# Kernel optimization log

Hardware: AMD Instinct MI355X
Metric: run time of the kernel (lower is better)

## Reference

```python
import jax, jax.numpy as jnp
import numpy as np

D_MODEL = 1024
NUM_HEADS = 16
D_K = D_MODEL // NUM_HEADS
THETA = 10000.0
B, S = 2, 2048
MAX_LEN = 2048


def precompute_cos_sin(head_dim, max_len, theta):
    # (max_len, head_dim): first half cos, second half sin, over head_dim//2 freqs
    freqs = 1.0 / theta ** (jnp.arange(0, head_dim, 2, dtype=jnp.float32) / head_dim)
    ang = jnp.arange(max_len, dtype=jnp.float32)[:, None] * freqs[None, :]  # (L, d/2)
    return jnp.concatenate([jnp.cos(ang), jnp.sin(ang)], axis=-1)  # (L, d)


def apply_rope(x, cos_sin):
    # x: (b, h, s, d); cos_sin: (b, 1, s, d) with cos|sin halves of size d//2
    x1 = x[..., 0::2]
    x2 = x[..., 1::2]
    cos, sin = jnp.split(cos_sin, 2, axis=-1)
    out = jnp.stack([x1 * cos - x2 * sin, x1 * sin + x2 * cos], axis=-1)
    return out.reshape(x.shape)


def setup_inputs() -> dict:
    key = jax.random.key(0)
    ks = jax.random.split(key, 6)
    std = np.sqrt(2.0 / (D_MODEL + D_MODEL))
    x = jax.random.normal(ks[0], (B, S, D_MODEL), dtype=jnp.float32)
    token_positions = jnp.sort(
        jax.random.randint(ks[1], (B, S), 0, MAX_LEN, dtype=jnp.int32), axis=-1)
    Wq = jax.random.normal(ks[2], (D_MODEL, D_MODEL), dtype=jnp.float32) * std
    Wk = jax.random.normal(ks[3], (D_MODEL, D_MODEL), dtype=jnp.float32) * std
    Wv = jax.random.normal(ks[4], (D_MODEL, D_MODEL), dtype=jnp.float32) * std
    Wo = jax.random.normal(ks[5], (D_MODEL, D_MODEL), dtype=jnp.float32) * std
    return {"x": x, "token_positions": token_positions,
            "Wq": Wq, "Wk": Wk, "Wv": Wv, "Wo": Wo}


def reference(x, token_positions, Wq, Wk, Wv, Wo):
    b, s, d = x.shape
    h, dk = NUM_HEADS, D_K
    # projections: weight is (out, in)
    Q = jnp.einsum('btd,od->bto', x, Wq).reshape(b, s, h, dk).transpose(0, 2, 1, 3)
    K = jnp.einsum('btd,od->bto', x, Wk).reshape(b, s, h, dk).transpose(0, 2, 1, 3)
    V = jnp.einsum('btd,od->bto', x, Wv).reshape(b, s, h, dk).transpose(0, 2, 1, 3)
    # RoPE
    cos_sin = precompute_cos_sin(dk, MAX_LEN, THETA)  # (L, dk)
    cs = cos_sin[token_positions][:, None, :, :]  # (b, 1, s, dk)
    Q = apply_rope(Q, cs)
    K = apply_rope(K, cs)
    # causal attention with full score matrix, as in the original
    scores = jnp.einsum('bhqd,bhkd->bhqk', Q, K) / jnp.sqrt(jnp.float32(dk))
    causal = jnp.tril(jnp.ones((s, s), dtype=bool))
    scores = jnp.where(causal[None, None], scores, -jnp.inf)
    weights = jax.nn.softmax(scores, axis=-1)
    out = jnp.einsum('bhqk,bhkd->bhqd', weights, V)
    out = out.transpose(0, 2, 1, 3).reshape(b, s, h * dk)
    return jnp.einsum('btd,od->bto', out, Wo)
```

## Files before the change

kernel.cpp:

```cpp
#include <hip/hip_runtime.h>
#include <math.h>

#define D_MODEL 1024
#define NHEADS  16
#define DK      64
#define BB      2
#define SS      2048
#define MT      (BB*SS)

typedef _Float16 half8 __attribute__((ext_vector_type(8)));
typedef _Float16 half4 __attribute__((ext_vector_type(4)));
typedef float f32x4 __attribute__((ext_vector_type(4)));

__global__ void rope_table_kernel(float* __restrict__ tab) {
    int idx = blockIdx.x * 256 + threadIdx.x;
    int p = idx >> 5;
    int i = idx & 31;
    float freq = powf(10000.0f, -(float)(2 * i) / 64.0f);
    float ang = (float)p * freq;
    tab[p * 64 + i]      = cosf(ang);
    tab[p * 64 + 32 + i] = sinf(ang);
}

__global__ __launch_bounds__(256) void gemm_awt_f16(
    const float* __restrict__ A,
    const float* __restrict__ W0, const float* __restrict__ W1, const float* __restrict__ W2,
    float* __restrict__ C0, float* __restrict__ C1, float* __restrict__ C2)
{
    const float* W;
    float* C;
    if (blockIdx.z == 0)      { W = W0; C = C0; }
    else if (blockIdx.z == 1) { W = W1; C = C1; }
    else                      { W = W2; C = C2; }

    __shared__ __align__(16) _Float16 Ah[128][40];
    __shared__ __align__(16) _Float16 Wh[64][40];

    int tid = threadIdx.x;
    int m0 = blockIdx.y * 128;
    int n0 = blockIdx.x * 64;

    int wid  = tid >> 6;
    int lane = tid & 63;
    int lm   = lane & 15;
    int lk   = (lane >> 4) * 8;
    int wm   = (wid & 1) * 64;
    int wn   = (wid >> 1) * 32;

    int ar = tid >> 1;
    int ah = (tid & 1) * 16;

    const float* ApBase = A + (size_t)(m0 + ar) * D_MODEL + ah;
    const float* WpBase = W + (size_t)(n0 + (ar & 63)) * D_MODEL + ah;

    f32x4 acc[4][2];
#pragma unroll
    for (int fm = 0; fm < 4; ++fm)
#pragma unroll
        for (int fn = 0; fn < 2; ++fn)
            acc[fm][fn] = (f32x4){0.f, 0.f, 0.f, 0.f};

    float4 ra[4], rw[4];
#pragma unroll
    for (int u = 0; u < 4; ++u) ra[u] = *(const float4*)(ApBase + u * 4);
    if (tid < 128) {
#pragma unroll
        for (int u = 0; u < 4; ++u) rw[u] = *(const float4*)(WpBase + u * 4);
    }

    for (int ks = 0; ks < 32; ++ks) {
        __syncthreads();
#pragma unroll
        for (int u = 0; u < 4; ++u) {
            float4 v = ra[u];
            half4 hv = {(_Float16)v.x, (_Float16)v.y, (_Float16)v.z, (_Float16)v.w};
            *(half4*)&Ah[ar][ah + u * 4] = hv;
        }
        if (tid < 128) {
#pragma unroll
            for (int u = 0; u < 4; ++u) {
                float4 v = rw[u];
                half4 hv = {(_Float16)v.x, (_Float16)v.y, (_Float16)v.z, (_Float16)v.w};
                *(half4*)&Wh[ar][ah + u * 4] = hv;
            }
        }
        __syncthreads();

        if (ks < 31) {
            int k0n = (ks + 1) * 32;
#pragma unroll
            for (int u = 0; u < 4; ++u) ra[u] = *(const float4*)(ApBase + k0n + u * 4);
            if (tid < 128) {
#pragma unroll
                for (int u = 0; u < 4; ++u) rw[u] = *(const float4*)(WpBase + k0n + u * 4);
            }
        }

        half8 af[4], bf[2];
#pragma unroll
        for (int fm = 0; fm < 4; ++fm) af[fm] = *(half8*)&Ah[wm + fm * 16 + lm][lk];
#pragma unroll
        for (int fn = 0; fn < 2; ++fn) bf[fn] = *(half8*)&Wh[wn + fn * 16 + lm][lk];
#pragma unroll
        for (int fm = 0; fm < 4; ++fm)
#pragma unroll
            for (int fn = 0; fn < 2; ++fn)
                acc[fm][fn] = __builtin_amdgcn_mfma_f32_16x16x32_f16(af[fm], bf[fn], acc[fm][fn], 0, 0, 0);
    }

    int fq = lane >> 4, fr = lane & 15;
#pragma unroll
    for (int fm = 0; fm < 4; ++fm)
#pragma unroll
        for (int fn = 0; fn < 2; ++fn) {
            float* Cp = C + (size_t)(m0 + wm + fm * 16 + fq * 4) * D_MODEL + n0 + wn + fn * 16 + fr;
#pragma unroll
            for (int r = 0; r < 4; ++r)
                Cp[(size_t)r * D_MODEL] = acc[fm][fn][r];
        }
}

__global__ void rope_apply_kernel(float* __restrict__ Qp, float* __restrict__ Kp,
                                  const int* __restrict__ pos, const float* __restrict__ tab)
{
    int idx = blockIdx.x * 256 + threadIdx.x;
    float* base = blockIdx.y ? Kp : Qp;
    int i = idx & 31;
    int row = idx >> 5;
    float* ptr = base + (size_t)row * 64 + 2 * i;
    int p = pos[idx >> 9];
    float c  = tab[p * 64 + i];
    float sn = tab[p * 64 + 32 + i];
    float2 v = *(float2*)ptr;
    float2 r;
    r.x = v.x * c - v.y * sn;
    r.y = v.x * sn + v.y * c;
    *(float2*)ptr = r;
}

__global__ __launch_bounds__(256) void attn_mfma_f16(
    const float* __restrict__ Q, const float* __restrict__ K,
    const float* __restrict__ V, float* __restrict__ O)
{
    __shared__ __align__(16) _Float16 Kh[64][72];
    __shared__ __align__(16) _Float16 Vt[64][72];
    __shared__ __align__(16) _Float16 Ph[64][72];

    int tid = threadIdx.x;
    int wid = tid >> 6;
    int lane = tid & 63;
    int fr = lane & 15;
    int fq = lane >> 4;
    int qbase = wid * 16;

    int bh = blockIdx.y;
    int b = bh >> 4, h = bh & 15;

    const float* Qb = Q + (size_t)b * SS * D_MODEL + h * DK;
    const float* Kb = K + (size_t)b * SS * D_MODEL + h * DK;
    const float* Vb = V + (size_t)b * SS * D_MODEL + h * DK;
    float* Ob = O + (size_t)b * SS * D_MODEL + h * DK;

    int sr = tid >> 4;
    int sc4 = (tid & 15) << 2;

#pragma unroll 1
    for (int half = 0; half < 2; ++half) {
        int qt = half ? (31 - blockIdx.x) : blockIdx.x;
        int q0 = qt * 64;

        half8 qf[2];
#pragma unroll
        for (int ks = 0; ks < 2; ++ks) {
            const float* qp = Qb + (size_t)(q0 + qbase + fr) * D_MODEL + ks * 32 + fq * 8;
            float4 a = *(const float4*)qp;
            float4 b2 = *(const float4*)(qp + 4);
            qf[ks] = (half8){(_Float16)a.x, (_Float16)a.y, (_Float16)a.z, (_Float16)a.w,
                             (_Float16)b2.x, (_Float16)b2.y, (_Float16)b2.z, (_Float16)b2.w};
        }

        float m[4], l[4];
        f32x4 oacc[4];
#pragma unroll
        for (int r = 0; r < 4; ++r) { m[r] = -1e30f; l[r] = 0.0f; }
#pragma unroll
        for (int fn = 0; fn < 4; ++fn) oacc[fn] = (f32x4){0.f, 0.f, 0.f, 0.f};

        float4 kv[4], vv[4];
#pragma unroll
        for (int u = 0; u < 4; ++u) {
            int r = u * 16 + sr;
            kv[u] = *(const float4*)(Kb + (size_t)r * D_MODEL + sc4);
            vv[u] = *(const float4*)(Vb + (size_t)r * D_MODEL + sc4);
        }

        for (int kt = 0; kt <= qt; ++kt) {
            __syncthreads();
#pragma unroll
            for (int u = 0; u < 4; ++u) {
                int r = u * 16 + sr;
                float4 k4 = kv[u];
                *(half4*)&Kh[r][sc4] = (half4){(_Float16)k4.x, (_Float16)k4.y, (_Float16)k4.z, (_Float16)k4.w};
                float4 v4 = vv[u];
                Vt[sc4 + 0][r] = (_Float16)v4.x;
                Vt[sc4 + 1][r] = (_Float16)v4.y;
                Vt[sc4 + 2][r] = (_Float16)v4.z;
                Vt[sc4 + 3][r] = (_Float16)v4.w;
            }
            __syncthreads();

            if (kt < qt) {
                int k0n = (kt + 1) * 64;
#pragma unroll
                for (int u = 0; u < 4; ++u) {
                    int r = u * 16 + sr;
                    kv[u] = *(const float4*)(Kb + (size_t)(k0n + r) * D_MODEL + sc4);
                    vv[u] = *(const float4*)(Vb + (size_t)(k0n + r) * D_MODEL + sc4);
                }
            }

            f32x4 sacc[4];
#pragma unroll
            for (int fn = 0; fn < 4; ++fn) sacc[fn] = (f32x4){0.f, 0.f, 0.f, 0.f};
#pragma unroll
            for (int ks = 0; ks < 2; ++ks) {
#pragma unroll
                for (int fn = 0; fn < 4; ++fn) {
                    half8 kf = *(half8*)&Kh[fn * 16 + fr][ks * 32 + fq * 8];
                    sacc[fn] = __builtin_amdgcn_mfma_f32_16x16x32_f16(qf[ks], kf, sacc[fn], 0, 0, 0);
                }
            }

            const float sc2 = 0.125f;
            float sv[4][4];
#pragma unroll
            for (int fn = 0; fn < 4; ++fn)
#pragma unroll
                for (int r = 0; r < 4; ++r) sv[fn][r] = sacc[fn][r] * sc2;
            if (kt == qt) {
#pragma unroll
                for (int fn = 0; fn < 4; ++fn)
#pragma unroll
                    for (int r = 0; r < 4; ++r)
                        if (fn * 16 + fr > qbase + fq * 4 + r) sv[fn][r] = -1e30f;
            }

            float p[4][4];
#pragma unroll
            for (int r = 0; r < 4; ++r) {
                float rm = fmaxf(fmaxf(sv[0][r], sv[1][r]), fmaxf(sv[2][r], sv[3][r]));
                rm = fmaxf(rm, __shfl_xor(rm, 1));
                rm = fmaxf(rm, __shfl_xor(rm, 2));
                rm = fmaxf(rm, __shfl_xor(rm, 4));
                rm = fmaxf(rm, __shfl_xor(rm, 8));
                float nm = fmaxf(m[r], rm);
                float alpha = __expf(m[r] - nm);
                m[r] = nm;
                float rs = 0.0f;
#pragma unroll
                for (int fn = 0; fn < 4; ++fn) { p[fn][r] = __expf(sv[fn][r] - nm); rs += p[fn][r]; }
                rs += __shfl_xor(rs, 1);
                rs += __shfl_xor(rs, 2);
                rs += __shfl_xor(rs, 4);
                rs += __shfl_xor(rs, 8);
                l[r] = l[r] * alpha + rs;
#pragma unroll
                for (int fn = 0; fn < 4; ++fn) oacc[fn][r] *= alpha;
            }

#pragma unroll
            for (int r = 0; r < 4; ++r)
#pragma unroll
                for (int fn = 0; fn < 4; ++fn)
                    Ph[qbase + fq * 4 + r][fn * 16 + fr] = (_Float16)p[fn][r];

#pragma unroll
            for (int ks = 0; ks < 2; ++ks) {
                half8 pa = *(half8*)&Ph[qbase + fr][ks * 32 + fq * 8];
#pragma unroll
                for (int fn = 0; fn < 4; ++fn) {
                    half8 vb = *(half8*)&Vt[fn * 16 + fr][ks * 32 + fq * 8];
                    oacc[fn] = __builtin_amdgcn_mfma_f32_16x16x32_f16(pa, vb, oacc[fn], 0, 0, 0);
                }
            }
        }

#pragma unroll
        for (int r = 0; r < 4; ++r) {
            float inv = 1.0f / l[r];
            size_t rowoff = (size_t)(q0 + qbase + fq * 4 + r) * D_MODEL;
#pragma unroll
            for (int fn = 0; fn < 4; ++fn)
                Ob[rowoff + fn * 16 + fr] = oacc[fn][r] * inv;
        }
    }
}

extern "C" void kernel_launch(void* const* d_in, const int* in_sizes, int n_in,
                              void* d_out, int out_size, void* d_ws, size_t ws_size,
                              hipStream_t stream)
{
    const float* x    = (const float*)d_in[0];
    const int*   tpos = (const int*)d_in[1];
    const float* Wq   = (const float*)d_in[2];
    const float* Wk   = (const float*)d_in[3];
    const float* Wv   = (const float*)d_in[4];
    const float* Wo   = (const float*)d_in[5];
    float* out = (float*)d_out;

    float* ws = (float*)d_ws;
    float* q   = ws;
    float* k   = q + (size_t)MT * D_MODEL;
    float* v   = k + (size_t)MT * D_MODEL;
    float* o   = v + (size_t)MT * D_MODEL;
    float* tab = o + (size_t)MT * D_MODEL;

    hipLaunchKernelGGL(rope_table_kernel, dim3(256), dim3(256), 0, stream, tab);
    hipLaunchKernelGGL(gemm_awt_f16, dim3(16, 32, 3), dim3(256), 0, stream,
                       x, Wq, Wk, Wv, q, k, v);
    hipLaunchKernelGGL(rope_apply_kernel, dim3(8192, 2), dim3(256), 0, stream,
                       q, k, tpos, tab);
    hipLaunchKernelGGL(attn_mfma_f16, dim3(16, 32), dim3(256), 0, stream,
                       q, k, v, o);
    hipLaunchKernelGGL(gemm_awt_f16, dim3(16, 32, 1), dim3(256), 0, stream,
                       o, Wo, Wo, Wo, out, out, out);
}
```

Before: 305.6 us.

## Pre-convert inputs and weights to fp16 and feed fp16 operands to GEMMs

Adds a conversion kernel that casts x and all four weight matrices to fp16 once per call. The GEMM now loads half-precision data directly, uses a 64-wide K tile with twice the MFMA work per sync, and has all threads share the weight tile load. Attention writes its output in fp16 into the reused x buffer, so the output projection reads half the bytes. This trades an extra pass over the inputs and weights for lower GEMM bandwidth, fewer in-loop conversions and fewer barriers.

```diff
diff --git a/kernel.cpp b/kernel.cpp
--- a/kernel.cpp
+++ b/kernel.cpp
@@ -22,19 +22,45 @@
     tab[p * 64 + 32 + i] = sinf(ang);
 }
 
-__global__ __launch_bounds__(256) void gemm_awt_f16(
-    const float* __restrict__ A,
-    const float* __restrict__ W0, const float* __restrict__ W1, const float* __restrict__ W2,
+__global__ __launch_bounds__(256) void cvt_f16_kernel(
+    const float* __restrict__ x,
+    const float* __restrict__ Wq, const float* __restrict__ Wk,
+    const float* __restrict__ Wv, const float* __restrict__ Wo,
+    _Float16* __restrict__ xh, _Float16* __restrict__ wh)
+{
+    size_t idx8 = ((size_t)blockIdx.x * 256 + threadIdx.x) * 8;
+    const float* src;
+    _Float16* dst;
+    if (idx8 < (size_t)4194304) {
+        src = x + idx8;
+        dst = xh + idx8;
+    } else {
+        size_t r = idx8 - 4194304;
+        int wi = (int)(r >> 20);
+        size_t off = r & 1048575;
+        src = (wi == 0 ? Wq : wi == 1 ? Wk : wi == 2 ? Wv : Wo) + off;
+        dst = wh + ((size_t)wi << 20) + off;
+    }
+    float4 a = *(const float4*)src;
+    float4 b = *(const float4*)(src + 4);
+    half8 h = {(_Float16)a.x, (_Float16)a.y, (_Float16)a.z, (_Float16)a.w,
+               (_Float16)b.x, (_Float16)b.y, (_Float16)b.z, (_Float16)b.w};
+    *(half8*)dst = h;
+}
+
+__global__ __launch_bounds__(256) void gemm_h(
+    const _Float16* __restrict__ A,
+    const _Float16* __restrict__ W0, const _Float16* __restrict__ W1, const _Float16* __restrict__ W2,
     float* __restrict__ C0, float* __restrict__ C1, float* __restrict__ C2)
 {
-    const float* W;
+    const _Float16* W;
     float* C;
     if (blockIdx.z == 0)      { W = W0; C = C0; }
     else if (blockIdx.z == 1) { W = W1; C = C1; }
     else                      { W = W2; C = C2; }
 
-    __shared__ __align__(16) _Float16 Ah[128][40];
-    __shared__ __align__(16) _Float16 Wh[64][40];
+    __shared__ __align__(16) _Float16 Ah[128][72];
+    __shared__ __align__(16) _Float16 Wh2[64][72];
 
     int tid = threadIdx.x;
     int m0 = blockIdx.y * 128;
@@ -48,10 +74,12 @@
     int wn   = (wid >> 1) * 32;
 
     int ar = tid >> 1;
-    int ah = (tid & 1) * 16;
-
-    const float* ApBase = A + (size_t)(m0 + ar) * D_MODEL + ah;
-    const float* WpBase = W + (size_t)(n0 + (ar & 63)) * D_MODEL + ah;
+    int ac = (tid & 1) * 32;
+    int wr = tid >> 2;
+    int wc = (tid & 3) * 16;
+
+    const _Float16* Ap = A + (size_t)(m0 + ar) * D_MODEL + ac;
+    const _Float16* Wp = W + (size_t)(n0 + wr) * D_MODEL + wc;
 
     f32x4 acc[4][2];
 #pragma unroll
@@ -60,52 +88,41 @@
         for (int fn = 0; fn < 2; ++fn)
             acc[fm][fn] = (f32x4){0.f, 0.f, 0.f, 0.f};
 
-    float4 ra[4], rw[4];
-#pragma unroll
-    for (int u = 0; u < 4; ++u) ra[u] = *(const float4*)(ApBase + u * 4);
-    if (tid < 128) {
-#pragma unroll
-        for (int u = 0; u < 4; ++u) rw[u] = *(const float4*)(WpBase + u * 4);
-    }
-
-    for (int ks = 0; ks < 32; ++ks) {
+    half8 ra[4], rw[2];
+#pragma unroll
+    for (int u = 0; u < 4; ++u) ra[u] = *(const half8*)(Ap + u * 8);
+#pragma unroll
+    for (int u = 0; u < 2; ++u) rw[u] = *(const half8*)(Wp + u * 8);
+
+    for (int ks = 0; ks < 16; ++ks) {
         __syncthreads();
 #pragma unroll
-        for (int u = 0; u < 4; ++u) {
-            float4 v = ra[u];
-            half4 hv = {(_Float16)v.x, (_Float16)v.y, (_Float16)v.z, (_Float16)v.w};
-            *(half4*)&Ah[ar][ah + u * 4] = hv;
-        }
-        if (tid < 128) {
-#pragma unroll
-            for (int u = 0; u < 4; ++u) {
-                float4 v = rw[u];
-                half4 hv = {(_Float16)v.x, (_Float16)v.y, (_Float16)v.z, (_Float16)v.w};
-                *(half4*)&Wh[ar][ah + u * 4] = hv;
-            }
-        }
+        for (int u = 0; u < 4; ++u) *(half8*)&Ah[ar][ac + u * 8] = ra[u];
+#pragma unroll
+        for (int u = 0; u < 2; ++u) *(half8*)&Wh2[wr][wc + u * 8] = rw[u];
         __syncthreads();
 
-        if (ks < 31) {
-            int k0n = (ks + 1) * 32;
-#pragma unroll
-            for (int u = 0; u < 4; ++u) ra[u] = *(const float4*)(ApBase + k0n + u * 4);
-            if (tid < 128) {
-#pragma unroll
-                for (int u = 0; u < 4; ++u) rw[u] = *(const float4*)(WpBase + k0n + u * 4);
-            }
-        }
-
-        half8 af[4], bf[2];
-#pragma unroll
-        for (int fm = 0; fm < 4; ++fm) af[fm] = *(half8*)&Ah[wm + fm * 16 + lm][lk];
-#pragma unroll
-        for (int fn = 0; fn < 2; ++fn) bf[fn] = *(half8*)&Wh[wn + fn * 16 + lm][lk];
-#pragma unroll
-        for (int fm = 0; fm < 4; ++fm)
-#pragma unroll
-            for (int fn = 0; fn < 2; ++fn)
-                acc[fm][fn] = __builtin_amdgcn_mfma_f32_16x16x32_f16(af[fm], bf[fn], acc[fm][fn], 0, 0, 0);
+        if (ks < 15) {
+            int k0n = (ks + 1) * 64;
+#pragma unroll
+            for (int u = 0; u < 4; ++u) ra[u] = *(const half8*)(Ap + k0n + u * 8);
+#pragma unroll
+            for (int u = 0; u < 2; ++u) rw[u] = *(const half8*)(Wp + k0n + u * 8);
+        }
+
+#pragma unroll
+        for (int kk = 0; kk < 2; ++kk) {
+            half8 af[4], bf[2];
+#pragma unroll
+            for (int fm = 0; fm < 4; ++fm) af[fm] = *(half8*)&Ah[wm + fm * 16 + lm][kk * 32 + lk];
+#pragma unroll
+            for (int fn = 0; fn < 2; ++fn) bf[fn] = *(half8*)&Wh2[wn + fn * 16 + lm][kk * 32 + lk];
+#pragma unroll
+            for (int fm = 0; fm < 4; ++fm)
+#pragma unroll
+                for (int fn = 0; fn < 2; ++fn)
+                    acc[fm][fn] = __builtin_amdgcn_mfma_f32_16x16x32_f16(af[fm], bf[fn], acc[fm][fn], 0, 0, 0);
+        }
     }
 
     int fq = lane >> 4, fr = lane & 15;
@@ -140,7 +157,7 @@
 
 __global__ __launch_bounds__(256) void attn_mfma_f16(
     const float* __restrict__ Q, const float* __restrict__ K,
-    const float* __restrict__ V, float* __restrict__ O)
+    const float* __restrict__ V, _Float16* __restrict__ O)
 {
     __shared__ __align__(16) _Float16 Kh[64][72];
     __shared__ __align__(16) _Float16 Vt[64][72];
@@ -159,7 +176,7 @@
     const float* Qb = Q + (size_t)b * SS * D_MODEL + h * DK;
     const float* Kb = K + (size_t)b * SS * D_MODEL + h * DK;
     const float* Vb = V + (size_t)b * SS * D_MODEL + h * DK;
-    float* Ob = O + (size_t)b * SS * D_MODEL + h * DK;
+    _Float16* Ob = O + (size_t)b * SS * D_MODEL + h * DK;
 
     int sr = tid >> 4;
     int sc4 = (tid & 15) << 2;
@@ -291,7 +308,7 @@
             size_t rowoff = (size_t)(q0 + qbase + fq * 4 + r) * D_MODEL;
 #pragma unroll
             for (int fn = 0; fn < 4; ++fn)
-                Ob[rowoff + fn * 16 + fr] = oacc[fn][r] * inv;
+                Ob[rowoff + fn * 16 + fr] = (_Float16)(oacc[fn][r] * inv);
         }
     }
 }
@@ -308,20 +325,23 @@
     const float* Wo   = (const float*)d_in[5];
     float* out = (float*)d_out;
 
-    float* ws = (float*)d_ws;
-    float* q   = ws;
-    float* k   = q + (size_t)MT * D_MODEL;
-    float* v   = k + (size_t)MT * D_MODEL;
-    float* o   = v + (size_t)MT * D_MODEL;
-    float* tab = o + (size_t)MT * D_MODEL;
-
+    float* q = (float*)d_ws;
+    float* k = q + (size_t)MT * D_MODEL;
+    float* v = k + (size_t)MT * D_MODEL;
+    _Float16* xoh = (_Float16*)(v + (size_t)MT * D_MODEL);
+    _Float16* wh  = xoh + (size_t)MT * D_MODEL;
+    float* tab = (float*)(wh + (size_t)MT * D_MODEL);
+
+    hipLaunchKernelGGL(cvt_f16_kernel, dim3(4096), dim3(256), 0, stream,
+                       x, Wq, Wk, Wv, Wo, xoh, wh);
     hipLaunchKernelGGL(rope_table_kernel, dim3(256), dim3(256), 0, stream, tab);
-    hipLaunchKernelGGL(gemm_awt_f16, dim3(16, 32, 3), dim3(256), 0, stream,
-                       x, Wq, Wk, Wv, q, k, v);
+    hipLaunchKernelGGL(gemm_h, dim3(16, 32, 3), dim3(256), 0, stream,
+                       xoh, wh, wh + (1u << 20), wh + (2u << 20), q, k, v);
     hipLaunchKernelGGL(rope_apply_kernel, dim3(8192, 2), dim3(256), 0, stream,
                        q, k, tpos, tab);
     hipLaunchKernelGGL(attn_mfma_f16, dim3(16, 32), dim3(256), 0, stream,
-                       q, k, v, o);
-    hipLaunchKernelGGL(gemm_awt_f16, dim3(16, 32, 1), dim3(256), 0, stream,
-                       o, Wo, Wo, Wo, out, out, out);
-}
+                       q, k, v, xoh);
+    hipLaunchKernelGGL(gemm_h, dim3(16, 32, 1), dim3(256), 0, stream,
+                       xoh, wh + (3u << 20), wh + (3u << 20), wh + (3u << 20),
+                       out, out, out);
+}
```

New measurement: 255.2 us. -16.5%, faster.
